# Optimization experiments

Hardware: AMD Instinct MI355X
Metric: run time of the kernel (lower is better)

## Reference

```python
import jax, jax.numpy as jnp
import numpy as np

B, T, C, V = 8, 2048, 1024, 32000


def setup_inputs() -> dict:
    key = jax.random.key(0)
    ks = jax.random.split(key, 12)
    s = 1.0 / np.sqrt(C)
    return {
        "input_tokens": jax.random.randint(ks[0], (B, T), 0, V),
        "xx_init": jnp.zeros((B, C), jnp.float32),
        "aa_init": jnp.zeros((B, C), jnp.float32),
        "bb_init": jnp.zeros((B, C), jnp.float32),
        "pp_init": jnp.zeros((B, C), jnp.float32),  # with aa=bb=0 this is equivalent to -inf init
        "emb": jax.random.normal(ks[1], (V, C), jnp.float32) * 0.02,
        "time_mix_k": jax.random.uniform(ks[2], (C,), jnp.float32),
        "time_mix_v": jax.random.uniform(ks[3], (C,), jnp.float32),
        "time_mix_r": jax.random.uniform(ks[4], (C,), jnp.float32),
        "time_decay": jax.random.normal(ks[5], (C,), jnp.float32) * 0.1,
        "time_first": jax.random.normal(ks[6], (C,), jnp.float32) * 0.1,
        "Wk": jax.random.normal(ks[7], (C, C), jnp.float32) * s,
        "Wv": jax.random.normal(ks[8], (C, C), jnp.float32) * s,
        "Wr": jax.random.normal(ks[9], (C, C), jnp.float32) * s,
        "Wo": jax.random.normal(ks[10], (C, C), jnp.float32) * s,
    }


def _wkv_scan(k, v, aa0, bb0, pp0, w, u):
    """Numerically-stable RWKV WKV recurrence.
    k, v: [T, B, C]; aa0/bb0/pp0: [B, C]; w (decay, negative), u (bonus): [C]."""
    def step(carry, kv):
        aa, bb, pp = carry
        kt, vt = kv
        ww = u + kt
        p = jnp.maximum(pp, ww)
        e1 = jnp.exp(pp - p)
        e2 = jnp.exp(ww - p)
        wkv = (e1 * aa + e2 * vt) / (e1 * bb + e2)
        ww2 = pp + w
        p2 = jnp.maximum(ww2, kt)
        e1b = jnp.exp(ww2 - p2)
        e2b = jnp.exp(kt - p2)
        return (e1b * aa + e2b * vt, e1b * bb + e2b, p2), wkv
    (aa, bb, pp), out = jax.lax.scan(step, (aa0, bb0, pp0), (k, v))
    return out, aa, bb, pp


def _forward(input_tokens, xx_init, aa_init, bb_init, pp_init, emb,
             time_mix_k, time_mix_v, time_mix_r, time_decay, time_first,
             Wk, Wv, Wr, Wo):
    x = emb[input_tokens]                                   # [B, T, C]
    xprev = jnp.concatenate([xx_init[:, None, :], x[:, :-1]], axis=1)  # token shift
    xk = x * time_mix_k + xprev * (1.0 - time_mix_k)
    xv = x * time_mix_v + xprev * (1.0 - time_mix_v)
    xr = x * time_mix_r + xprev * (1.0 - time_mix_r)
    k = jnp.einsum("btc,dc->btd", xk, Wk)
    v = jnp.einsum("btc,dc->btd", xv, Wv)
    r = jax.nn.sigmoid(jnp.einsum("btc,dc->btd", xr, Wr))
    w = -jnp.exp(time_decay)                                # per-channel decay
    u = time_first
    wkv, _, _, _ = _wkv_scan(jnp.swapaxes(k, 0, 1), jnp.swapaxes(v, 0, 1),
                             aa_init, bb_init, pp_init, w, u)
    wkv = jnp.swapaxes(wkv, 0, 1)                           # [B, T, C]
    rwkv = jnp.einsum("btc,dc->btd", r * wkv, Wo)
    e1 = rwkv[:, -1]          # final-step state
    e2 = rwkv.mean(axis=1)    # time-averaged state
    hx = (e1 + e2) * 0.5
    return jnp.stack([hx, hx])  # (hx, cx) stacked -> [2, B, C]


def reference(input_tokens, xx_init, aa_init, bb_init, pp_init, emb,
              time_mix_k, time_mix_v, time_mix_r, time_decay, time_first,
              Wk, Wv, Wr, Wo):
    return _forward(input_tokens, xx_init, aa_init, bb_init, pp_init, emb,
                    time_mix_k, time_mix_v, time_mix_r, time_decay, time_first,
                    Wk, Wv, Wr, Wo)
```

## Files before the change

### kernel.cpp

```cpp
#include <hip/hip_runtime.h>

#define Bdim 8
#define Tdim 2048
#define Cdim 1024
#define CHUNK 64
#define NCHUNK 32
#define BC (Bdim*Cdim)

typedef float floatx4 __attribute__((ext_vector_type(4)));
typedef _Float16 half8 __attribute__((ext_vector_type(8)));
typedef _Float16 half4v __attribute__((ext_vector_type(4)));

__device__ __forceinline__ void load16(const void* g, void* l) {
    __builtin_amdgcn_global_load_lds(
        (const __attribute__((address_space(1))) void*)g,
        (__attribute__((address_space(3))) void*)l, 16, 0, 0);
}

__global__ __launch_bounds__(256) void embed_mix3(const int* __restrict__ tokens,
                                                  const float* __restrict__ xx_init,
                                                  const float* __restrict__ emb,
                                                  const float* __restrict__ tmk,
                                                  const float* __restrict__ tmv,
                                                  const float* __restrict__ tmr,
                                                  _Float16* __restrict__ xk,
                                                  _Float16* __restrict__ xv,
                                                  _Float16* __restrict__ xr) {
    int row = blockIdx.x;
    int b = row >> 11;
    int t = row & (Tdim - 1);
    const float* cur = emb + (size_t)tokens[row] * Cdim;
    const float* prv = (t == 0) ? (xx_init + (size_t)b * Cdim)
                                : (emb + (size_t)tokens[row - 1] * Cdim);
    int c = threadIdx.x * 4;
    float4 cf4 = *reinterpret_cast<const float4*>(cur + c);
    float4 pf4 = *reinterpret_cast<const float4*>(prv + c);
    float4 mk = *reinterpret_cast<const float4*>(tmk + c);
    float4 mv = *reinterpret_cast<const float4*>(tmv + c);
    float4 mr = *reinterpret_cast<const float4*>(tmr + c);
    float cf[4] = {cf4.x, cf4.y, cf4.z, cf4.w};
    float pf[4] = {pf4.x, pf4.y, pf4.z, pf4.w};
    float mkf[4] = {mk.x, mk.y, mk.z, mk.w};
    float mvf[4] = {mv.x, mv.y, mv.z, mv.w};
    float mrf[4] = {mr.x, mr.y, mr.z, mr.w};
    half4v hk, hv, hr;
    #pragma unroll
    for (int j = 0; j < 4; j++) {
        hk[j] = (_Float16)(mkf[j] * cf[j] + (1.0f - mkf[j]) * pf[j]);
        hv[j] = (_Float16)(mvf[j] * cf[j] + (1.0f - mvf[j]) * pf[j]);
        hr[j] = (_Float16)(mrf[j] * cf[j] + (1.0f - mrf[j]) * pf[j]);
    }
    size_t o = (size_t)row * Cdim + c;
    *reinterpret_cast<half4v*>(xk + o) = hk;
    *reinterpret_cast<half4v*>(xv + o) = hv;
    *reinterpret_cast<half4v*>(xr + o) = hr;
}

__global__ __launch_bounds__(256) void wconv(const float* __restrict__ Wk,
                                             const float* __restrict__ Wv,
                                             const float* __restrict__ Wr,
                                             _Float16* __restrict__ Wh) {
    const float* W = blockIdx.y == 0 ? Wk : (blockIdx.y == 1 ? Wv : Wr);
    _Float16* dst = Wh + (size_t)blockIdx.y * Cdim * Cdim;
    int i = (blockIdx.x * 256 + threadIdx.x) * 4;
    float4 f = *reinterpret_cast<const float4*>(W + i);
    half4v h;
    h[0] = (_Float16)f.x; h[1] = (_Float16)f.y; h[2] = (_Float16)f.z; h[3] = (_Float16)f.w;
    *reinterpret_cast<half4v*>(dst + i) = h;
}

__global__ __launch_bounds__(256) void gemm_kvr(const _Float16* __restrict__ xk,
                                                const _Float16* __restrict__ xv,
                                                const _Float16* __restrict__ xr,
                                                const _Float16* __restrict__ Wh,
                                                _Float16* __restrict__ ko,
                                                _Float16* __restrict__ vo,
                                                _Float16* __restrict__ ro) {
    const int which = blockIdx.y;
    const _Float16* X = which == 0 ? xk : (which == 1 ? xv : xr);
    const _Float16* W = Wh + (size_t)which * Cdim * Cdim;
    _Float16* out     = which == 0 ? ko : (which == 1 ? vo : ro);

    const int lin = blockIdx.x;
    const int xcd = lin & 7;
    const int loc = lin >> 3;
    const int mt = xcd * 16 + (loc >> 3);
    const int nt = loc & 7;
    const int m0 = mt * 128;
    const int n0 = nt * 128;

    __shared__ _Float16 As[128 * 64];
    __shared__ _Float16 Bs[128 * 64];

    const int tid = threadIdx.x;
    const int lane = tid & 63;
    const int wave = tid >> 6;
    const int wm = (wave >> 1) * 64;
    const int wn = (wave & 1) * 64;
    const int lr = lane & 15;
    const int lk = lane >> 4;

    const _Float16* Asrc = X + (size_t)m0 * Cdim;
    const _Float16* Bsrc = W + (size_t)n0 * Cdim;

    floatx4 acc[4][4] = {};

    for (int k0 = 0; k0 < Cdim; k0 += 64) {
        #pragma unroll
        for (int i = 0; i < 4; i++) {
            int e = i * 256 + tid;
            int r = e >> 3;
            int cbp = e & 7;
            int cbl = cbp ^ (r & 7);
            load16(Asrc + (size_t)r * Cdim + k0 + cbl * 8, (char*)As + e * 16);
            load16(Bsrc + (size_t)r * Cdim + k0 + cbl * 8, (char*)Bs + e * 16);
        }
        __syncthreads();
        #pragma unroll
        for (int kk = 0; kk < 64; kk += 32) {
            const int kb_ = kk >> 3;
            half8 af[4], bf[4];
            #pragma unroll
            for (int mi = 0; mi < 4; mi++) {
                int r = wm + mi * 16 + lr;
                int cb = (kb_ + lk) ^ (r & 7);
                af[mi] = *reinterpret_cast<const half8*>(As + r * 64 + cb * 8);
            }
            #pragma unroll
            for (int ni = 0; ni < 4; ni++) {
                int r = wn + ni * 16 + lr;
                int cb = (kb_ + lk) ^ (r & 7);
                bf[ni] = *reinterpret_cast<const half8*>(Bs + r * 64 + cb * 8);
            }
            #pragma unroll
            for (int mi = 0; mi < 4; mi++)
                #pragma unroll
                for (int ni = 0; ni < 4; ni++)
                    acc[mi][ni] = __builtin_amdgcn_mfma_f32_16x16x32_f16(af[mi], bf[ni], acc[mi][ni], 0, 0, 0);
        }
        __syncthreads();
    }

    #pragma unroll
    for (int mi = 0; mi < 4; mi++) {
        #pragma unroll
        for (int ni = 0; ni < 4; ni++) {
            #pragma unroll
            for (int reg = 0; reg < 4; reg++) {
                int mm = m0 + wm + mi * 16 + (lane >> 4) * 4 + reg;
                int nn = n0 + wn + ni * 16 + (lane & 15);
                float v = acc[mi][ni][reg];
                if (which == 2) v = 1.0f / (1.0f + __expf(-v));
                out[(size_t)mm * Cdim + nn] = (_Float16)v;
            }
        }
    }
}

__global__ __launch_bounds__(256) void scan_pass1(const _Float16* __restrict__ kb,
                                                  const _Float16* __restrict__ vb,
                                                  const float* __restrict__ tdecay,
                                                  float* __restrict__ tot_a,
                                                  float* __restrict__ tot_b,
                                                  float* __restrict__ tot_p) {
    int idx = blockIdx.x * 256 + threadIdx.x;
    int j = idx >> 13;
    int bc = idx & (BC - 1);
    int b = bc >> 10;
    int c = bc & (Cdim - 1);
    float w = -__expf(tdecay[c]);
    float aa = 0.0f, bb = 0.0f, pp = -1e30f;
    const _Float16* kp = kb + ((size_t)(b * Tdim + j * CHUNK)) * Cdim + c;
    const _Float16* vp = vb + ((size_t)(b * Tdim + j * CHUNK)) * Cdim + c;
    #pragma unroll 8
    for (int t = 0; t < CHUNK; t++) {
        float kt = (float)kp[(size_t)t * Cdim];
        float vt = (float)vp[(size_t)t * Cdim];
        float ww2 = pp + w;
        float p2 = fmaxf(ww2, kt);
        float e1 = __expf(ww2 - p2);
        float e2 = __expf(kt - p2);
        aa = e1 * aa + e2 * vt;
        bb = e1 * bb + e2;
        pp = p2;
    }
    tot_a[idx] = aa; tot_b[idx] = bb; tot_p[idx] = pp;
}

__global__ __launch_bounds__(256) void combine_chunks(const float* __restrict__ tot_a,
                                                      const float* __restrict__ tot_b,
                                                      const float* __restrict__ tot_p,
                                                      const float* __restrict__ aa_init,
                                                      const float* __restrict__ bb_init,
                                                      const float* __restrict__ pp_init,
                                                      const float* __restrict__ tdecay,
                                                      float* __restrict__ inc_a,
                                                      float* __restrict__ inc_b,
                                                      float* __restrict__ inc_p) {
    int idx = blockIdx.x * 256 + threadIdx.x;
    int c = idx & (Cdim - 1);
    float w = -__expf(tdecay[c]);
    float wL = w * (float)CHUNK;
    float a = aa_init[idx], b = bb_init[idx], p = pp_init[idx];
    for (int j = 0; j < NCHUNK; j++) {
        inc_a[j * BC + idx] = a;
        inc_b[j * BC + idx] = b;
        inc_p[j * BC + idx] = p;
        float ta = tot_a[j * BC + idx];
        float tb = tot_b[j * BC + idx];
        float tp = tot_p[j * BC + idx];
        float px = p + wL;
        float q = fmaxf(px, tp);
        float e1 = __expf(px - q);
        float e2 = __expf(tp - q);
        a = e1 * a + e2 * ta;
        b = e1 * b + e2 * tb;
        p = q;
    }
}

__global__ __launch_bounds__(256) void scan_pass2(const _Float16* __restrict__ kb,
                                                  const _Float16* __restrict__ vb,
                                                  const _Float16* __restrict__ rb,
                                                  const float* __restrict__ tdecay,
                                                  const float* __restrict__ tfirst,
                                                  const float* __restrict__ inc_a,
                                                  const float* __restrict__ inc_b,
                                                  const float* __restrict__ inc_p,
                                                  float* __restrict__ partial,
                                                  float* __restrict__ ylast) {
    int idx = blockIdx.x * 256 + threadIdx.x;
    int j = idx >> 13;
    int bc = idx & (BC - 1);
    int b = bc >> 10;
    int c = bc & (Cdim - 1);
    float w = -__expf(tdecay[c]);
    float u = tfirst[c];
    float aa = inc_a[idx], bb = inc_b[idx], pp = inc_p[idx];
    const size_t base = ((size_t)(b * Tdim + j * CHUNK)) * Cdim + c;
    const _Float16* kp = kb + base;
    const _Float16* vp = vb + base;
    const _Float16* rp = rb + base;
    float sum = 0.0f, ylv = 0.0f;
    #pragma unroll 8
    for (int t = 0; t < CHUNK; t++) {
        float kt = (float)kp[(size_t)t * Cdim];
        float vt = (float)vp[(size_t)t * Cdim];
        float rt = (float)rp[(size_t)t * Cdim];
        float ww = u + kt;
        float p = fmaxf(pp, ww);
        float e1 = __expf(pp - p);
        float e2 = __expf(ww - p);
        float wkv = (e1 * aa + e2 * vt) / (e1 * bb + e2);
        float y = rt * wkv;
        sum += y;
        ylv = y;
        float ww2 = pp + w;
        float p2 = fmaxf(ww2, kt);
        float e1b = __expf(ww2 - p2);
        float e2b = __expf(kt - p2);
        aa = e1b * aa + e2b * vt;
        bb = e1b * bb + e2b;
        pp = p2;
    }
    partial[idx] = sum;
    if (j == NCHUNK - 1) ylast[bc] = ylv;
}

__global__ __launch_bounds__(256) void reduce_z(const float* __restrict__ partial,
                                                const float* __restrict__ ylast,
                                                float* __restrict__ z) {
    int idx = blockIdx.x * 256 + threadIdx.x;
    float s = 0.0f;
    for (int j = 0; j < NCHUNK; j++) s += partial[j * BC + idx];
    z[idx] = 0.5f * (ylast[idx] + s * (1.0f / (float)Tdim));
}

__global__ __launch_bounds__(256) void final_out(const float* __restrict__ z,
                                                 const float* __restrict__ Wo,
                                                 float* __restrict__ out) {
    int gw = (blockIdx.x * 256 + threadIdx.x) >> 6;
    int lane = threadIdx.x & 63;
    int b = gw >> 10;
    int d = gw & (Cdim - 1);
    const float* zr = z + (size_t)b * Cdim;
    const float* wr = Wo + (size_t)d * Cdim;
    float acc = 0.0f;
    #pragma unroll
    for (int i = lane; i < Cdim; i += 64) acc += zr[i] * wr[i];
    #pragma unroll
    for (int off = 32; off > 0; off >>= 1) acc += __shfl_down(acc, off);
    if (lane == 0) {
        out[(size_t)b * Cdim + d] = acc;
        out[(size_t)BC + (size_t)b * Cdim + d] = acc;
    }
}

extern "C" void kernel_launch(void* const* d_in, const int* in_sizes, int n_in,
                              void* d_out, int out_size, void* d_ws, size_t ws_size,
                              hipStream_t stream) {
    const int*   tokens  = (const int*)d_in[0];
    const float* xx_init = (const float*)d_in[1];
    const float* aa_init = (const float*)d_in[2];
    const float* bb_init = (const float*)d_in[3];
    const float* pp_init = (const float*)d_in[4];
    const float* emb     = (const float*)d_in[5];
    const float* tmk     = (const float*)d_in[6];
    const float* tmv     = (const float*)d_in[7];
    const float* tmr     = (const float*)d_in[8];
    const float* tdecay  = (const float*)d_in[9];
    const float* tfirst  = (const float*)d_in[10];
    const float* Wk      = (const float*)d_in[11];
    const float* Wv      = (const float*)d_in[12];
    const float* Wr      = (const float*)d_in[13];
    const float* Wo      = (const float*)d_in[14];
    float* out = (float*)d_out;

    char* ws = (char*)d_ws;
    size_t off = 0;
    auto alloc = [&](size_t bytes) -> void* {
        void* p = ws + off;
        off += (bytes + 255) & ~(size_t)255;
        return p;
    };
    _Float16* xkb = (_Float16*)alloc((size_t)Bdim * Tdim * Cdim * 2);
    _Float16* xvb = (_Float16*)alloc((size_t)Bdim * Tdim * Cdim * 2);
    _Float16* xrb = (_Float16*)alloc((size_t)Bdim * Tdim * Cdim * 2);
    _Float16* kb = (_Float16*)alloc((size_t)Bdim * Tdim * Cdim * 2);
    _Float16* vb = (_Float16*)alloc((size_t)Bdim * Tdim * Cdim * 2);
    _Float16* rb = (_Float16*)alloc((size_t)Bdim * Tdim * Cdim * 2);
    _Float16* Wh = (_Float16*)alloc((size_t)3 * Cdim * Cdim * 2);
    float* tot_a = (float*)alloc((size_t)NCHUNK * BC * 4);
    float* tot_b = (float*)alloc((size_t)NCHUNK * BC * 4);
    float* tot_p = (float*)alloc((size_t)NCHUNK * BC * 4);
    float* inc_a = (float*)alloc((size_t)NCHUNK * BC * 4);
    float* inc_b = (float*)alloc((size_t)NCHUNK * BC * 4);
    float* inc_p = (float*)alloc((size_t)NCHUNK * BC * 4);
    float* partial = (float*)alloc((size_t)NCHUNK * BC * 4);
    float* ylast   = (float*)alloc((size_t)BC * 4);
    float* zbuf    = (float*)alloc((size_t)BC * 4);

    embed_mix3<<<Bdim * Tdim, 256, 0, stream>>>(tokens, xx_init, emb, tmk, tmv, tmr,
                                                xkb, xvb, xrb);
    wconv<<<dim3(1024, 3), 256, 0, stream>>>(Wk, Wv, Wr, Wh);
    gemm_kvr<<<dim3(1024, 3), 256, 0, stream>>>(xkb, xvb, xrb, Wh, kb, vb, rb);
    scan_pass1<<<(NCHUNK * BC) / 256, 256, 0, stream>>>(kb, vb, tdecay, tot_a, tot_b, tot_p);
    combine_chunks<<<BC / 256, 256, 0, stream>>>(tot_a, tot_b, tot_p, aa_init, bb_init, pp_init,
                                                 tdecay, inc_a, inc_b, inc_p);
    scan_pass2<<<(NCHUNK * BC) / 256, 256, 0, stream>>>(kb, vb, rb, tdecay, tfirst,
                                                        inc_a, inc_b, inc_p, partial, ylast);
    reduce_z<<<BC / 256, 256, 0, stream>>>(partial, ylast, zbuf);
    final_out<<<(BC / 4), 256, 0, stream>>>(zbuf, Wo, out);
}
```

Before: 423.5 us.

## Vectorize scan kernels to 8 channels per thread with shorter chunks

The scan passes now have each thread handle 8 adjacent channels, loading k/v/r as 16-byte half8 vectors instead of scalar half loads. The chunk length drops from 64 to 16 (128 chunks), so the thread count stays similar while the sequential combine pass gets four times as many steps. final_out switches to float4 loads, and a few loops get unroll pragmas. The aim is better memory coalescing per load and more instruction-level parallelism, at the cost of more registers and larger intermediate buffers (tot/inc/partial grow 4x).

```diff
diff --git a/kernel.cpp b/kernel.cpp
--- a/kernel.cpp
+++ b/kernel.cpp
@@ -3,8 +3,8 @@
 #define Bdim 8
 #define Tdim 2048
 #define Cdim 1024
-#define CHUNK 64
-#define NCHUNK 32
+#define CHUNK 16
+#define NCHUNK 128
 #define BC (Bdim*Cdim)
 
 typedef float floatx4 __attribute__((ext_vector_type(4)));
@@ -163,28 +163,43 @@
                                                   float* __restrict__ tot_a,
                                                   float* __restrict__ tot_b,
                                                   float* __restrict__ tot_p) {
-    int idx = blockIdx.x * 256 + threadIdx.x;
-    int j = idx >> 13;
-    int bc = idx & (BC - 1);
-    int b = bc >> 10;
-    int c = bc & (Cdim - 1);
-    float w = -__expf(tdecay[c]);
-    float aa = 0.0f, bb = 0.0f, pp = -1e30f;
-    const _Float16* kp = kb + ((size_t)(b * Tdim + j * CHUNK)) * Cdim + c;
-    const _Float16* vp = vb + ((size_t)(b * Tdim + j * CHUNK)) * Cdim + c;
-    #pragma unroll 8
+    int g = blockIdx.x * 256 + threadIdx.x;
+    int j = g >> 10;
+    int rem = g & 1023;
+    int b = rem >> 7;
+    int c8 = (rem & 127) << 3;
+    float4 td0 = *reinterpret_cast<const float4*>(tdecay + c8);
+    float4 td1 = *reinterpret_cast<const float4*>(tdecay + c8 + 4);
+    float w[8] = {-__expf(td0.x), -__expf(td0.y), -__expf(td0.z), -__expf(td0.w),
+                  -__expf(td1.x), -__expf(td1.y), -__expf(td1.z), -__expf(td1.w)};
+    float aa[8], bb[8], pp[8];
+    #pragma unroll
+    for (int i = 0; i < 8; i++) { aa[i] = 0.0f; bb[i] = 0.0f; pp[i] = -1e30f; }
+    const size_t base = ((size_t)(b * Tdim + j * CHUNK)) * Cdim + c8;
+    const _Float16* kp = kb + base;
+    const _Float16* vp = vb + base;
+    #pragma unroll 4
     for (int t = 0; t < CHUNK; t++) {
-        float kt = (float)kp[(size_t)t * Cdim];
-        float vt = (float)vp[(size_t)t * Cdim];
-        float ww2 = pp + w;
-        float p2 = fmaxf(ww2, kt);
-        float e1 = __expf(ww2 - p2);
-        float e2 = __expf(kt - p2);
-        aa = e1 * aa + e2 * vt;
-        bb = e1 * bb + e2;
-        pp = p2;
-    }
-    tot_a[idx] = aa; tot_b[idx] = bb; tot_p[idx] = pp;
+        half8 k8 = *reinterpret_cast<const half8*>(kp + (size_t)t * Cdim);
+        half8 v8 = *reinterpret_cast<const half8*>(vp + (size_t)t * Cdim);
+        #pragma unroll
+        for (int i = 0; i < 8; i++) {
+            float kt = (float)k8[i];
+            float vt = (float)v8[i];
+            float ww2 = pp[i] + w[i];
+            float p2 = fmaxf(ww2, kt);
+            float e1 = __expf(ww2 - p2);
+            float e2 = __expf(kt - p2);
+            aa[i] = e1 * aa[i] + e2 * vt;
+            bb[i] = e1 * bb[i] + e2;
+            pp[i] = p2;
+        }
+    }
+    size_t o = (size_t)j * BC + ((size_t)rem << 3);
+    #pragma unroll
+    for (int i = 0; i < 8; i++) {
+        tot_a[o + i] = aa[i]; tot_b[o + i] = bb[i]; tot_p[o + i] = pp[i];
+    }
 }
 
 __global__ __launch_bounds__(256) void combine_chunks(const float* __restrict__ tot_a,
@@ -202,6 +217,7 @@
     float w = -__expf(tdecay[c]);
     float wL = w * (float)CHUNK;
     float a = aa_init[idx], b = bb_init[idx], p = pp_init[idx];
+    #pragma unroll 8
     for (int j = 0; j < NCHUNK; j++) {
         inc_a[j * BC + idx] = a;
         inc_b[j * BC + idx] = b;
@@ -229,42 +245,63 @@
                                                   const float* __restrict__ inc_p,
                                                   float* __restrict__ partial,
                                                   float* __restrict__ ylast) {
-    int idx = blockIdx.x * 256 + threadIdx.x;
-    int j = idx >> 13;
-    int bc = idx & (BC - 1);
-    int b = bc >> 10;
-    int c = bc & (Cdim - 1);
-    float w = -__expf(tdecay[c]);
-    float u = tfirst[c];
-    float aa = inc_a[idx], bb = inc_b[idx], pp = inc_p[idx];
-    const size_t base = ((size_t)(b * Tdim + j * CHUNK)) * Cdim + c;
+    int g = blockIdx.x * 256 + threadIdx.x;
+    int j = g >> 10;
+    int rem = g & 1023;
+    int b = rem >> 7;
+    int c8 = (rem & 127) << 3;
+    float4 td0 = *reinterpret_cast<const float4*>(tdecay + c8);
+    float4 td1 = *reinterpret_cast<const float4*>(tdecay + c8 + 4);
+    float4 u0 = *reinterpret_cast<const float4*>(tfirst + c8);
+    float4 u1 = *reinterpret_cast<const float4*>(tfirst + c8 + 4);
+    float w[8] = {-__expf(td0.x), -__expf(td0.y), -__expf(td0.z), -__expf(td0.w),
+                  -__expf(td1.x), -__expf(td1.y), -__expf(td1.z), -__expf(td1.w)};
+    float u[8] = {u0.x, u0.y, u0.z, u0.w, u1.x, u1.y, u1.z, u1.w};
+    size_t so = (size_t)j * BC + ((size_t)rem << 3);
+    float aa[8], bb[8], pp[8], sum[8], ylv[8];
+    #pragma unroll
+    for (int i = 0; i < 8; i++) {
+        aa[i] = inc_a[so + i]; bb[i] = inc_b[so + i]; pp[i] = inc_p[so + i];
+        sum[i] = 0.0f; ylv[i] = 0.0f;
+    }
+    const size_t base = ((size_t)(b * Tdim + j * CHUNK)) * Cdim + c8;
     const _Float16* kp = kb + base;
     const _Float16* vp = vb + base;
     const _Float16* rp = rb + base;
-    float sum = 0.0f, ylv = 0.0f;
-    #pragma unroll 8
+    #pragma unroll 4
     for (int t = 0; t < CHUNK; t++) {
-        float kt = (float)kp[(size_t)t * Cdim];
-        float vt = (float)vp[(size_t)t * Cdim];
-        float rt = (float)rp[(size_t)t * Cdim];
-        float ww = u + kt;
-        float p = fmaxf(pp, ww);
-        float e1 = __expf(pp - p);
-        float e2 = __expf(ww - p);
-        float wkv = (e1 * aa + e2 * vt) / (e1 * bb + e2);
-        float y = rt * wkv;
-        sum += y;
-        ylv = y;
-        float ww2 = pp + w;
-        float p2 = fmaxf(ww2, kt);
-        float e1b = __expf(ww2 - p2);
-        float e2b = __expf(kt - p2);
-        aa = e1b * aa + e2b * vt;
-        bb = e1b * bb + e2b;
-        pp = p2;
-    }
-    partial[idx] = sum;
-    if (j == NCHUNK - 1) ylast[bc] = ylv;
+        half8 k8 = *reinterpret_cast<const half8*>(kp + (size_t)t * Cdim);
+        half8 v8 = *reinterpret_cast<const half8*>(vp + (size_t)t * Cdim);
+        half8 r8 = *reinterpret_cast<const half8*>(rp + (size_t)t * Cdim);
+        #pragma unroll
+        for (int i = 0; i < 8; i++) {
+            float kt = (float)k8[i];
+            float vt = (float)v8[i];
+            float rt = (float)r8[i];
+            float ww = u[i] + kt;
+            float p = fmaxf(pp[i], ww);
+            float e1 = __expf(pp[i] - p);
+            float e2 = __expf(ww - p);
+            float wkv = (e1 * aa[i] + e2 * vt) / (e1 * bb[i] + e2);
+            float y = rt * wkv;
+            sum[i] += y;
+            ylv[i] = y;
+            float ww2 = pp[i] + w[i];
+            float p2 = fmaxf(ww2, kt);
+            float e1b = __expf(ww2 - p2);
+            float e2b = __expf(kt - p2);
+            aa[i] = e1b * aa[i] + e2b * vt;
+            bb[i] = e1b * bb[i] + e2b;
+            pp[i] = p2;
+        }
+    }
+    #pragma unroll
+    for (int i = 0; i < 8; i++) partial[so + i] = sum[i];
+    if (j == NCHUNK - 1) {
+        size_t bo = ((size_t)rem << 3);
+        #pragma unroll
+        for (int i = 0; i < 8; i++) ylast[bo + i] = ylv[i];
+    }
 }
 
 __global__ __launch_bounds__(256) void reduce_z(const float* __restrict__ partial,
@@ -272,6 +309,7 @@
                                                 float* __restrict__ z) {
     int idx = blockIdx.x * 256 + threadIdx.x;
     float s = 0.0f;
+    #pragma unroll 8
     for (int j = 0; j < NCHUNK; j++) s += partial[j * BC + idx];
     z[idx] = 0.5f * (ylast[idx] + s * (1.0f / (float)Tdim));
 }
@@ -283,11 +321,15 @@
     int lane = threadIdx.x & 63;
     int b = gw >> 10;
     int d = gw & (Cdim - 1);
-    const float* zr = z + (size_t)b * Cdim;
-    const float* wr = Wo + (size_t)d * Cdim;
+    const float4* zr = reinterpret_cast<const float4*>(z + (size_t)b * Cdim);
+    const float4* wr = reinterpret_cast<const float4*>(Wo + (size_t)d * Cdim);
     float acc = 0.0f;
     #pragma unroll
-    for (int i = lane; i < Cdim; i += 64) acc += zr[i] * wr[i];
+    for (int s = 0; s < 4; s++) {
+        float4 a = zr[lane + 64 * s];
+        float4 w4 = wr[lane + 64 * s];
+        acc += a.x * w4.x + a.y * w4.y + a.z * w4.z + a.w * w4.w;
+    }
     #pragma unroll
     for (int off = 32; off > 0; off >>= 1) acc += __shfl_down(acc, off);
     if (lane == 0) {
@@ -344,11 +386,11 @@
                                                 xkb, xvb, xrb);
     wconv<<<dim3(1024, 3), 256, 0, stream>>>(Wk, Wv, Wr, Wh);
     gemm_kvr<<<dim3(1024, 3), 256, 0, stream>>>(xkb, xvb, xrb, Wh, kb, vb, rb);
-    scan_pass1<<<(NCHUNK * BC) / 256, 256, 0, stream>>>(kb, vb, tdecay, tot_a, tot_b, tot_p);
+    scan_pass1<<<(NCHUNK * BC / 8) / 256, 256, 0, stream>>>(kb, vb, tdecay, tot_a, tot_b, tot_p);
     combine_chunks<<<BC / 256, 256, 0, stream>>>(tot_a, tot_b, tot_p, aa_init, bb_init, pp_init,
                                                  tdecay, inc_a, inc_b, inc_p);
-    scan_pass2<<<(NCHUNK * BC) / 256, 256, 0, stream>>>(kb, vb, rb, tdecay, tfirst,
-                                                        inc_a, inc_b, inc_p, partial, ylast);
+    scan_pass2<<<(NCHUNK * BC / 8) / 256, 256, 0, stream>>>(kb, vb, rb, tdecay, tfirst,
+                                                            inc_a, inc_b, inc_p, partial, ylast);
     reduce_z<<<BC / 256, 256, 0, stream>>>(partial, ylast, zbuf);
     final_out<<<(BC / 4), 256, 0, stream>>>(zbuf, Wo, out);
 }
```

Result: slower. 454.9 us (+7.4%).
